# Optimization experiments

Measured on AMD Instinct MI355X. Metric: run time of the kernel, lower is better.

## Reference

```python
import jax, jax.numpy as jnp
import numpy as np


def setup_inputs() -> dict:
    key = jax.random.key(0)
    k1, k2, k3 = jax.random.split(key, 3)
    B, L, D, K = 64, 1024, 768, 1024
    token_embeddings = jax.random.normal(k1, (B, L, D), dtype=jnp.float32)
    gates = jax.random.uniform(k2, (B, L), dtype=jnp.float32)
    attention_mask = jnp.ones((B, L), dtype=jnp.float32)
    centroids = jax.random.normal(k3, (K, D), dtype=jnp.float32)
    return {
        "token_embeddings": token_embeddings,
        "gates": gates,
        "attention_mask": attention_mask,
        "centroids": centroids,
        "entity_cluster": 0,
    }


def reference(token_embeddings, gates, attention_mask, centroids, entity_cluster):
    # ClusterFilter.apply: cdist -> argmin -> entity-cluster gating mask
    B, L, D = token_embeddings.shape
    flat = token_embeddings.reshape(-1, D)                      # [B*L, D]
    # squared Euclidean distances (argmin is invariant to sqrt)
    x2 = jnp.sum(flat * flat, axis=-1, keepdims=True)           # [B*L, 1]
    c2 = jnp.sum(centroids * centroids, axis=-1)                # [K]
    d2 = x2 - 2.0 * (flat @ centroids.T) + c2                   # [B*L, K]
    assignments = jnp.argmin(d2, axis=1).reshape(B, L)          # [B, L]
    entity_mask = (assignments == entity_cluster).astype(gates.dtype)
    entity_mask = entity_mask * attention_mask
    return gates * entity_mask
```

## Files before the change

### kernel.cpp

```cpp
#include <hip/hip_runtime.h>
#include <hip/hip_bf16.h>
#include <stdint.h>

typedef _Float16 half_t;
typedef __attribute__((ext_vector_type(8))) _Float16 half8;
typedef __attribute__((ext_vector_type(4))) _Float16 half4v;
typedef __attribute__((ext_vector_type(4))) float float4v;
typedef unsigned long long u64;

#define D_DIM 768
#define K_CENT 1024
#define M_TOTAL 65536
#define BM 256
#define BN 256
#define BK 32
#define NT 24
#define NTN 4

#define BPLANE 16384u

#define CLO_OFF  (NTN * NT * BPLANE)
#define C2_OFF   (2u * CLO_OFF)
#define PART_OFF (C2_OFF + 8192u)


__device__ __forceinline__ uint32_t swz(uint32_t row, uint32_t kbyte) {
  return (row * 64u + kbyte) ^ (((row >> 1) & 3u) << 4);
}

__device__ __forceinline__ void gll16(const void* g, void* l) {
  __builtin_amdgcn_global_load_lds((const __attribute__((address_space(1))) void*)g,
                                   (__attribute__((address_space(3))) void*)l,
                                   16, 0, 0);
}

__global__ __launch_bounds__(256) void prep_centroids(const float* __restrict__ cent,
                                                      uint8_t* __restrict__ ws) {
  const int n = blockIdx.x;
  const int nt = n >> 8, row = n & 255;
  float ss = 0.f;
  for (int d = threadIdx.x; d < D_DIM; d += 256) {
    float a = cent[n * D_DIM + d];
    ss += a * a;
    half_t hi = (half_t)a;
    half_t lo = (half_t)(a - (float)hi);
    int chunk = d >> 5, k = d & 31;
    uint32_t off = (uint32_t)(nt * NT + chunk) * BPLANE + swz((uint32_t)row, (uint32_t)k * 2u);
    *(half_t*)(ws + off) = hi;
    *(half_t*)(ws + CLO_OFF + off) = lo;
  }
  for (int s = 32; s > 0; s >>= 1) ss += __shfl_down(ss, s, 64);
  __shared__ float red[4];
  if ((threadIdx.x & 63) == 0) red[threadIdx.x >> 6] = ss;
  __syncthreads();
  if (threadIdx.x == 0) {
    float* c2 = (float*)(ws + C2_OFF);
    c2[n] = red[0] + red[1] + red[2] + red[3];
  }
}

__global__ __launch_bounds__(512, 2) void cluster_gemm(const float* __restrict__ X,
                                                       const uint8_t* __restrict__ wsro,
                                                       u64* __restrict__ partial) {
  extern __shared__ uint8_t smem[];

  const int bid = blockIdx.x;
  const int L = (bid & 7) * 128 + (bid >> 3);
  const int m_tile = L >> 2, n_tile = L & 3;
  const int m0 = m_tile * BM;

  const int tid = threadIdx.x;
  const int lane = tid & 63, w = tid >> 6;
  const int wm = w >> 2, wn = w & 3;
  const uint32_t kb = (uint32_t)((lane >> 4) << 4);

  const float* c2p = (const float*)(wsro + C2_OFF);
  const int ncol = n_tile * 256 + wn * 64 + (lane & 15);
  float c2v[4];
#pragma unroll
  for (int n = 0; n < 4; ++n) c2v[n] = c2p[ncol + n * 16];

  float4v acc[8][4];
#pragma unroll
  for (int m = 0; m < 8; ++m)
#pragma unroll
    for (int n = 0; n < 4; ++n) acc[m][n] = (float4v){0.f, 0.f, 0.f, 0.f};

  float4v apf[4];
  half8 ah[4], al[4], bh0[2], bl0[2], bh1[2], bl1[2];

#define A_LOAD(T1) { const int d0 = (T1) * BK;                                        \
  _Pragma("unroll") for (int i = 0; i < 4; ++i) {                                     \
    int f = tid + i * 512; int row = f >> 3, c4 = f & 7;                              \
    apf[i] = *(const float4v*)(X + (size_t)(m0 + row) * D_DIM + d0 + c4 * 4); } }

#define A_WRITE(DB) { _Pragma("unroll") for (int i = 0; i < 4; ++i) {                 \
    int f = tid + i * 512; int row = f >> 3, c4 = f & 7;                              \
    half4v hi, lo;                                                                    \
    _Pragma("unroll") for (int j = 0; j < 4; ++j) {                                   \
      half_t h = (half_t)apf[i][j]; hi[j] = h; lo[j] = (half_t)(apf[i][j] - (float)h);} \
    uint32_t a = (DB) + swz((uint32_t)row, (uint32_t)c4 * 8u);                        \
    *(half4v*)(smem + a) = hi; *(half4v*)(smem + a + 16384u) = lo; } }

#define B_GLL_HI(T1, DB) { const uint8_t* s_ = wsro + (uint32_t)(n_tile * NT + (T1)) * BPLANE; \
    uint32_t o_ = (uint32_t)w * 2048u;                                                \
    gll16(s_ + o_ + (lane << 4), smem + (DB) + o_);                                   \
    gll16(s_ + o_ + 1024u + (lane << 4), smem + (DB) + o_ + 1024u); }

#define B_GLL_LO(T1, DB) { const uint8_t* s_ = wsro + CLO_OFF + (uint32_t)(n_tile * NT + (T1)) * BPLANE; \
    uint32_t o_ = (uint32_t)w * 2048u;                                                \
    gll16(s_ + o_ + (lane << 4), smem + (DB) + 16384u + o_);                          \
    gll16(s_ + o_ + 1024u + (lane << 4), smem + (DB) + 16384u + o_ + 1024u); }

#define READ_A(HALF, AB) { _Pragma("unroll") for (int m = 0; m < 4; ++m) {            \
    uint32_t a = (AB) + swz((uint32_t)(wm * 128 + ((HALF) * 4 + m) * 16 + (lane & 15)), kb); \
    ah[m] = *(const half8*)(smem + a); al[m] = *(const half8*)(smem + a + 16384u); } }

#define READ_B(NH, BB, BH, BL) { _Pragma("unroll") for (int n = 0; n < 2; ++n) {      \
    uint32_t a = (BB) + swz((uint32_t)(wn * 64 + ((NH) * 2 + n) * 16 + (lane & 15)), kb); \
    BH[n] = *(const half8*)(smem + a); BL[n] = *(const half8*)(smem + a + 16384u); } }

#define MFMA_Q(MB, NB, BH, BL) { __builtin_amdgcn_s_setprio(1);                       \
  _Pragma("unroll") for (int m = 0; m < 4; ++m)                                       \
  _Pragma("unroll") for (int n = 0; n < 2; ++n) {                                     \
    float4v* A_ = &acc[(MB) + m][(NB) + n];                                           \
    *A_ = __builtin_amdgcn_mfma_f32_16x16x32_f16(ah[m], BH[n], *A_, 0, 0, 0);         \
    *A_ = __builtin_amdgcn_mfma_f32_16x16x32_f16(ah[m], BL[n], *A_, 0, 0, 0);         \
    *A_ = __builtin_amdgcn_mfma_f32_16x16x32_f16(al[m], BH[n], *A_, 0, 0, 0); }       \
  __builtin_amdgcn_s_setprio(0); }

#define BAR() __builtin_amdgcn_s_barrier()

  uint32_t Ab = 0u, Bb = 65536u;

  A_LOAD(0);
  B_GLL_HI(0, Bb); B_GLL_LO(0, Bb);
  A_WRITE(Ab);
  asm volatile("s_waitcnt vmcnt(0) lgkmcnt(0)" ::: "memory");
  BAR();

  for (int t = 0; t < NT; ++t) {
    const uint32_t AbN = Ab ^ 32768u, BbN = Bb ^ 32768u;
    const bool st = (t + 1 < NT);
    if (st) { A_LOAD(t + 1); B_GLL_HI(t + 1, BbN); }
    READ_A(0, Ab);
    READ_B(0, Bb, bh0, bl0);
    BAR();
    MFMA_Q(0, 0, bh0, bl0);
    BAR();
    if (st) { B_GLL_LO(t + 1, BbN); }
    READ_B(1, Bb, bh1, bl1);
    BAR();
    MFMA_Q(0, 2, bh1, bl1);
    BAR();
    READ_A(1, Ab);
    BAR();
    MFMA_Q(4, 2, bh1, bl1);
    BAR();
    if (st) { A_WRITE(AbN); }
    MFMA_Q(4, 0, bh0, bl0);
    asm volatile("s_waitcnt vmcnt(0) lgkmcnt(0)" ::: "memory");
    BAR();
    Ab = AbN; Bb = BbN;
  }

  u64* scratch = (u64*)smem;
  const int g = lane >> 4;
#pragma unroll
  for (int m = 0; m < 8; ++m) {
#pragma unroll
    for (int r = 0; r < 4; ++r) {
      u64 key = ~0ull;
#pragma unroll
      for (int n = 0; n < 4; ++n) {
        float s = c2v[n] - 2.0f * acc[m][n][r];
        uint32_t ub = __float_as_uint(s);
        ub ^= (uint32_t)((int32_t)ub >> 31) | 0x80000000u;
        u64 cand = ((u64)ub << 32) | (uint32_t)(ncol + n * 16);
        key = cand < key ? cand : key;
      }
#pragma unroll
      for (int d = 1; d < 16; d <<= 1) {
        u64 o = __shfl_xor(key, d, 64);
        key = o < key ? o : key;
      }
      if ((lane & 15) == 0) {
        int row = wm * 128 + m * 16 + g * 4 + r;
        scratch[row * 4 + wn] = key;
      }
    }
  }
  __syncthreads();
  if (tid < 256) {
    u64 k = scratch[tid * 4];
#pragma unroll
    for (int j = 1; j < 4; ++j) { u64 o = scratch[tid * 4 + j]; k = o < k ? o : k; }
    partial[(size_t)(m0 + tid) * NTN + n_tile] = k;
  }
}

__global__ __launch_bounds__(256) void finalize(const u64* __restrict__ partial,
                                                const float* __restrict__ gates,
                                                const float* __restrict__ att,
                                                const int* __restrict__ ecp,
                                                float* __restrict__ out) {
  int r = blockIdx.x * 256 + threadIdx.x;
  const u64* p = partial + (size_t)r * NTN;
  u64 k = p[0];
#pragma unroll
  for (int j = 1; j < NTN; ++j) { u64 o = p[j]; k = o < k ? o : k; }
  int idx = (int)(uint32_t)k;
  out[r] = gates[r] * att[r] * ((idx == *ecp) ? 1.0f : 0.0f);
}

extern "C" void kernel_launch(void* const* d_in, const int* in_sizes, int n_in,
                              void* d_out, int out_size, void* d_ws, size_t ws_size,
                              hipStream_t stream) {
  const float* X     = (const float*)d_in[0];
  const float* gates = (const float*)d_in[1];
  const float* att   = (const float*)d_in[2];
  const float* cent  = (const float*)d_in[3];
  const int*   ec    = (const int*)d_in[4];
  uint8_t* ws = (uint8_t*)d_ws;
  float* out = (float*)d_out;
  u64* partial = (u64*)(ws + PART_OFF);

  hipFuncSetAttribute((const void*)cluster_gemm,
                      hipFuncAttributeMaxDynamicSharedMemorySize, 131072);

  prep_centroids<<<K_CENT, 256, 0, stream>>>(cent, ws);
  cluster_gemm<<<(M_TOTAL / BM) * NTN, 512, 131072, stream>>>(X, ws, partial);
  finalize<<<M_TOTAL / 256, 256, 0, stream>>>(partial, gates, att, ec, out);
}
```

Baseline: 490.5 us.

## Pre-split X into fp16 hi/lo swizzled planes and stream via global_load_lds

```diff
diff --git a/kernel.cpp b/kernel.cpp
--- a/kernel.cpp
+++ b/kernel.cpp
@@ -22,7 +22,10 @@
 #define CLO_OFF  (NTN * NT * BPLANE)
 #define C2_OFF   (2u * CLO_OFF)
 #define PART_OFF (C2_OFF + 8192u)
-
+#define XHI_OFF  8388608u
+#define XPLANE   100663296u
+#define XLO_OFF  (XHI_OFF + XPLANE)
+#define WS_NEED  ((size_t)XLO_OFF + (size_t)XPLANE)
 
 __device__ __forceinline__ uint32_t swz(uint32_t row, uint32_t kbyte) {
   return (row * 64u + kbyte) ^ (((row >> 1) & 3u) << 4);
@@ -33,6 +36,8 @@
                                    (__attribute__((address_space(3))) void*)l,
                                    16, 0, 0);
 }
+
+#define BAR() __builtin_amdgcn_s_barrier()
 
 __global__ __launch_bounds__(256) void prep_centroids(const float* __restrict__ cent,
                                                       uint8_t* __restrict__ ws) {
@@ -59,15 +64,38 @@
   }
 }
 
-__global__ __launch_bounds__(512, 2) void cluster_gemm(const float* __restrict__ X,
-                                                       const uint8_t* __restrict__ wsro,
-                                                       u64* __restrict__ partial) {
+__global__ __launch_bounds__(256) void prep_x(const float* __restrict__ X,
+                                              uint8_t* __restrict__ ws) {
+  const uint32_t bid = blockIdx.x;
+  const uint32_t mt = bid / 24u, ch = bid % 24u;
+  const int tid = threadIdx.x;
+  const int row = tid >> 3, c4 = tid & 7;
+  const uint32_t pbase = (mt * 24u + ch) * BPLANE;
+#pragma unroll
+  for (int i = 0; i < 8; ++i) {
+    int r = row + i * 32;
+    float4v v = *(const float4v*)(X + (size_t)(mt * 256u + r) * D_DIM + ch * 32 + c4 * 4);
+    half4v hi, lo;
+#pragma unroll
+    for (int j = 0; j < 4; ++j) {
+      half_t h = (half_t)v[j];
+      hi[j] = h;
+      lo[j] = (half_t)(v[j] - (float)h);
+    }
+    uint32_t a = pbase + swz((uint32_t)r, (uint32_t)c4 * 8u);
+    *(half4v*)(ws + XHI_OFF + a) = hi;
+    *(half4v*)(ws + XLO_OFF + a) = lo;
+  }
+}
+
+__global__ __launch_bounds__(512, 2) void cluster_gemm_gl(const uint8_t* __restrict__ wsro,
+                                                          u64* __restrict__ partial) {
   extern __shared__ uint8_t smem[];
 
   const int bid = blockIdx.x;
   const int L = (bid & 7) * 128 + (bid >> 3);
-  const int m_tile = L >> 2, n_tile = L & 3;
-  const int m0 = m_tile * BM;
+  const int mt = L >> 2, nt = L & 3;
+  const int m0 = mt * BM;
 
   const int tid = threadIdx.x;
   const int lane = tid & 63, w = tid >> 6;
@@ -75,7 +103,7 @@
   const uint32_t kb = (uint32_t)((lane >> 4) << 4);
 
   const float* c2p = (const float*)(wsro + C2_OFF);
-  const int ncol = n_tile * 256 + wn * 64 + (lane & 15);
+  const int ncol = nt * 256 + wn * 64 + (lane & 15);
   float c2v[4];
 #pragma unroll
   for (int n = 0; n < 4; ++n) c2v[n] = c2p[ncol + n * 16];
@@ -86,38 +114,24 @@
 #pragma unroll
     for (int n = 0; n < 4; ++n) acc[m][n] = (float4v){0.f, 0.f, 0.f, 0.f};
 
-  float4v apf[4];
+  const uint8_t* Ah = wsro + XHI_OFF + (uint32_t)(mt * NT) * BPLANE;
+  const uint8_t* Al = wsro + XLO_OFF + (uint32_t)(mt * NT) * BPLANE;
+  const uint8_t* Bh = wsro + (uint32_t)(nt * NT) * BPLANE;
+  const uint8_t* Bl = wsro + CLO_OFF + (uint32_t)(nt * NT) * BPLANE;
+  const uint32_t wo = (uint32_t)w * 2048u;
+
   half8 ah[4], al[4], bh0[2], bl0[2], bh1[2], bl1[2];
 
-#define A_LOAD(T1) { const int d0 = (T1) * BK;                                        \
-  _Pragma("unroll") for (int i = 0; i < 4; ++i) {                                     \
-    int f = tid + i * 512; int row = f >> 3, c4 = f & 7;                              \
-    apf[i] = *(const float4v*)(X + (size_t)(m0 + row) * D_DIM + d0 + c4 * 4); } }
-
-#define A_WRITE(DB) { _Pragma("unroll") for (int i = 0; i < 4; ++i) {                 \
-    int f = tid + i * 512; int row = f >> 3, c4 = f & 7;                              \
-    half4v hi, lo;                                                                    \
-    _Pragma("unroll") for (int j = 0; j < 4; ++j) {                                   \
-      half_t h = (half_t)apf[i][j]; hi[j] = h; lo[j] = (half_t)(apf[i][j] - (float)h);} \
-    uint32_t a = (DB) + swz((uint32_t)row, (uint32_t)c4 * 8u);                        \
-    *(half4v*)(smem + a) = hi; *(half4v*)(smem + a + 16384u) = lo; } }
-
-#define B_GLL_HI(T1, DB) { const uint8_t* s_ = wsro + (uint32_t)(n_tile * NT + (T1)) * BPLANE; \
-    uint32_t o_ = (uint32_t)w * 2048u;                                                \
-    gll16(s_ + o_ + (lane << 4), smem + (DB) + o_);                                   \
-    gll16(s_ + o_ + 1024u + (lane << 4), smem + (DB) + o_ + 1024u); }
-
-#define B_GLL_LO(T1, DB) { const uint8_t* s_ = wsro + CLO_OFF + (uint32_t)(n_tile * NT + (T1)) * BPLANE; \
-    uint32_t o_ = (uint32_t)w * 2048u;                                                \
-    gll16(s_ + o_ + (lane << 4), smem + (DB) + 16384u + o_);                          \
-    gll16(s_ + o_ + 1024u + (lane << 4), smem + (DB) + 16384u + o_ + 1024u); }
-
-#define READ_A(HALF, AB) { _Pragma("unroll") for (int m = 0; m < 4; ++m) {            \
-    uint32_t a = (AB) + swz((uint32_t)(wm * 128 + ((HALF) * 4 + m) * 16 + (lane & 15)), kb); \
+#define GL_CP(SRC, DOFF) {                                                            \
+    gll16((SRC) + wo + (lane << 4), smem + (DOFF) + wo);                              \
+    gll16((SRC) + wo + 1024u + (lane << 4), smem + (DOFF) + wo + 1024u); }
+
+#define GL_RA(HALF, DB) { _Pragma("unroll") for (int m = 0; m < 4; ++m) {             \
+    uint32_t a = (DB) + swz((uint32_t)(wm * 128 + ((HALF) * 4 + m) * 16 + (lane & 15)), kb); \
     ah[m] = *(const half8*)(smem + a); al[m] = *(const half8*)(smem + a + 16384u); } }
 
-#define READ_B(NH, BB, BH, BL) { _Pragma("unroll") for (int n = 0; n < 2; ++n) {      \
-    uint32_t a = (BB) + swz((uint32_t)(wn * 64 + ((NH) * 2 + n) * 16 + (lane & 15)), kb); \
+#define GL_RB(NH, DB, BH, BL) { _Pragma("unroll") for (int n = 0; n < 2; ++n) {       \
+    uint32_t a = (DB) + 32768u + swz((uint32_t)(wn * 64 + ((NH) * 2 + n) * 16 + (lane & 15)), kb); \
     BH[n] = *(const half8*)(smem + a); BL[n] = *(const half8*)(smem + a + 16384u); } }
 
 #define MFMA_Q(MB, NB, BH, BL) { __builtin_amdgcn_s_setprio(1);                       \
@@ -129,7 +143,131 @@
     *A_ = __builtin_amdgcn_mfma_f32_16x16x32_f16(al[m], BH[n], *A_, 0, 0, 0); }       \
   __builtin_amdgcn_s_setprio(0); }
 
-#define BAR() __builtin_amdgcn_s_barrier()
+  GL_CP(Ah, 0u); GL_CP(Al, 16384u);
+  GL_CP(Bh, 32768u); GL_CP(Bl, 49152u);
+  asm volatile("s_waitcnt vmcnt(0)" ::: "memory");
+  BAR();
+
+  uint32_t cb = 0u;
+  for (int t = 0; t < NT; ++t) {
+    const uint32_t nb = cb ^ 65536u;
+    const bool st = (t + 1 < NT);
+    const uint32_t po = (uint32_t)(t + 1) * BPLANE;
+    if (st) { GL_CP(Ah + po, nb); GL_CP(Al + po, nb + 16384u); }
+    GL_RA(0, cb);
+    GL_RB(0, cb, bh0, bl0);
+    BAR();
+    MFMA_Q(0, 0, bh0, bl0);
+    BAR();
+    if (st) { GL_CP(Bh + po, nb + 32768u); GL_CP(Bl + po, nb + 49152u); }
+    GL_RB(1, cb, bh1, bl1);
+    BAR();
+    MFMA_Q(0, 2, bh1, bl1);
+    BAR();
+    GL_RA(1, cb);
+    BAR();
+    MFMA_Q(4, 2, bh1, bl1);
+    MFMA_Q(4, 0, bh0, bl0);
+    asm volatile("s_waitcnt vmcnt(0)" ::: "memory");
+    BAR();
+    cb = nb;
+  }
+
+  u64* scratch = (u64*)smem;
+  const int g = lane >> 4;
+#pragma unroll
+  for (int m = 0; m < 8; ++m) {
+#pragma unroll
+    for (int r = 0; r < 4; ++r) {
+      u64 key = ~0ull;
+#pragma unroll
+      for (int n = 0; n < 4; ++n) {
+        float s = c2v[n] - 2.0f * acc[m][n][r];
+        uint32_t ub = __float_as_uint(s);
+        ub ^= (uint32_t)((int32_t)ub >> 31) | 0x80000000u;
+        u64 cand = ((u64)ub << 32) | (uint32_t)(ncol + n * 16);
+        key = cand < key ? cand : key;
+      }
+#pragma unroll
+      for (int d = 1; d < 16; d <<= 1) {
+        u64 o = __shfl_xor(key, d, 64);
+        key = o < key ? o : key;
+      }
+      if ((lane & 15) == 0) {
+        int row = wm * 128 + m * 16 + g * 4 + r;
+        scratch[row * 4 + wn] = key;
+      }
+    }
+  }
+  __syncthreads();
+  if (tid < 256) {
+    u64 k = scratch[tid * 4];
+#pragma unroll
+    for (int j = 1; j < 4; ++j) { u64 o = scratch[tid * 4 + j]; k = o < k ? o : k; }
+    partial[(size_t)(m0 + tid) * NTN + nt] = k;
+  }
+}
+
+__global__ __launch_bounds__(512, 2) void cluster_gemm_rs(const float* __restrict__ X,
+                                                          const uint8_t* __restrict__ wsro,
+                                                          u64* __restrict__ partial) {
+  extern __shared__ uint8_t smem[];
+
+  const int bid = blockIdx.x;
+  const int L = (bid & 7) * 128 + (bid >> 3);
+  const int m_tile = L >> 2, n_tile = L & 3;
+  const int m0 = m_tile * BM;
+
+  const int tid = threadIdx.x;
+  const int lane = tid & 63, w = tid >> 6;
+  const int wm = w >> 2, wn = w & 3;
+  const uint32_t kb = (uint32_t)((lane >> 4) << 4);
+
+  const float* c2p = (const float*)(wsro + C2_OFF);
+  const int ncol = n_tile * 256 + wn * 64 + (lane & 15);
+  float c2v[4];
+#pragma unroll
+  for (int n = 0; n < 4; ++n) c2v[n] = c2p[ncol + n * 16];
+
+  float4v acc[8][4];
+#pragma unroll
+  for (int m = 0; m < 8; ++m)
+#pragma unroll
+    for (int n = 0; n < 4; ++n) acc[m][n] = (float4v){0.f, 0.f, 0.f, 0.f};
+
+  float4v apf[4];
+  half8 ah[4], al[4], bh0[2], bl0[2], bh1[2], bl1[2];
+
+#define A_LOAD(T1) { const int d0 = (T1) * BK;                                        \
+  _Pragma("unroll") for (int i = 0; i < 4; ++i) {                                     \
+    int f = tid + i * 512; int row = f >> 3, c4 = f & 7;                              \
+    apf[i] = *(const float4v*)(X + (size_t)(m0 + row) * D_DIM + d0 + c4 * 4); } }
+
+#define A_WRITE(DB) { _Pragma("unroll") for (int i = 0; i < 4; ++i) {                 \
+    int f = tid + i * 512; int row = f >> 3, c4 = f & 7;                              \
+    half4v hi, lo;                                                                    \
+    _Pragma("unroll") for (int j = 0; j < 4; ++j) {                                   \
+      half_t h = (half_t)apf[i][j]; hi[j] = h; lo[j] = (half_t)(apf[i][j] - (float)h);} \
+    uint32_t a = (DB) + swz((uint32_t)row, (uint32_t)c4 * 8u);                        \
+    *(half4v*)(smem + a) = hi; *(half4v*)(smem + a + 16384u) = lo; } }
+
+#define B_GLL_HI(T1, DB) { const uint8_t* s_ = wsro + (uint32_t)(n_tile * NT + (T1)) * BPLANE; \
+    uint32_t o_ = (uint32_t)w * 2048u;                                                \
+    gll16(s_ + o_ + (lane << 4), smem + (DB) + o_);                                   \
+    gll16(s_ + o_ + 1024u + (lane << 4), smem + (DB) + o_ + 1024u); }
+
+#define B_GLL_LO(T1, DB) { const uint8_t* s_ = wsro + CLO_OFF + (uint32_t)(n_tile * NT + (T1)) * BPLANE; \
+    uint32_t o_ = (uint32_t)w * 2048u;                                                \
+    gll16(s_ + o_ + (lane << 4), smem + (DB) + 16384u + o_);                          \
+    gll16(s_ + o_ + 1024u + (lane << 4), smem + (DB) + 16384u + o_ + 1024u); }
+
+#define READ_A(HALF, AB) { _Pragma("unroll") for (int m = 0; m < 4; ++m) {            \
+    uint32_t a = (AB) + swz((uint32_t)(wm * 128 + ((HALF) * 4 + m) * 16 + (lane & 15)), kb); \
+    ah[m] = *(const half8*)(smem + a); al[m] = *(const half8*)(smem + a + 16384u); } }
+
+#define READ_B(NH, BB, BH, BL) { _Pragma("unroll") for (int n = 0; n < 2; ++n) {      \
+    uint32_t a = (BB) + swz((uint32_t)(wn * 64 + ((NH) * 2 + n) * 16 + (lane & 15)), kb); \
+    BH[n] = *(const half8*)(smem + a); BL[n] = *(const half8*)(smem + a + 16384u); } }
 
   uint32_t Ab = 0u, Bb = 65536u;
 
@@ -225,10 +363,17 @@
   float* out = (float*)d_out;
   u64* partial = (u64*)(ws + PART_OFF);
 
-  hipFuncSetAttribute((const void*)cluster_gemm,
+  hipFuncSetAttribute((const void*)cluster_gemm_gl,
                       hipFuncAttributeMaxDynamicSharedMemorySize, 131072);
+  hipFuncSetAttribute((const void*)cluster_gemm_rs,
+                      hipFuncAttributeMaxDynamicSharedMemorySize, 131072);
 
   prep_centroids<<<K_CENT, 256, 0, stream>>>(cent, ws);
-  cluster_gemm<<<(M_TOTAL / BM) * NTN, 512, 131072, stream>>>(X, ws, partial);
+  if (ws_size >= WS_NEED) {
+    prep_x<<<256 * 24, 256, 0, stream>>>(X, ws);
+    cluster_gemm_gl<<<(M_TOTAL / BM) * NTN, 512, 131072, stream>>>(ws, partial);
+  } else {
+    cluster_gemm_rs<<<(M_TOTAL / BM) * NTN, 512, 131072, stream>>>(X, ws, partial);
+  }
   finalize<<<M_TOTAL / 256, 256, 0, stream>>>(partial, gates, att, ec, out);
 }
```

Result: slower. 564.2 us (+15.0%).

## Software-pipeline LDS fragment reads with MFMA and cut barriers per k-step

Applied to the files above, without the earlier changes.

```diff
diff --git a/kernel.cpp b/kernel.cpp
--- a/kernel.cpp
+++ b/kernel.cpp
@@ -33,6 +33,8 @@
                                    (__attribute__((address_space(3))) void*)l,
                                    16, 0, 0);
 }
+
+#define BAR() __builtin_amdgcn_s_barrier()
 
 __global__ __launch_bounds__(256) void prep_centroids(const float* __restrict__ cent,
                                                       uint8_t* __restrict__ ws) {
@@ -87,7 +89,7 @@
     for (int n = 0; n < 4; ++n) acc[m][n] = (float4v){0.f, 0.f, 0.f, 0.f};
 
   float4v apf[4];
-  half8 ah[4], al[4], bh0[2], bl0[2], bh1[2], bl1[2];
+  half8 ah0[4], al0[4], ah1[4], al1[4], bh0[2], bl0[2], bh1[2], bl1[2];
 
 #define A_LOAD(T1) { const int d0 = (T1) * BK;                                        \
   _Pragma("unroll") for (int i = 0; i < 4; ++i) {                                     \
@@ -112,24 +114,22 @@
     gll16(s_ + o_ + (lane << 4), smem + (DB) + 16384u + o_);                          \
     gll16(s_ + o_ + 1024u + (lane << 4), smem + (DB) + 16384u + o_ + 1024u); }
 
-#define READ_A(HALF, AB) { _Pragma("unroll") for (int m = 0; m < 4; ++m) {            \
-    uint32_t a = (AB) + swz((uint32_t)(wm * 128 + ((HALF) * 4 + m) * 16 + (lane & 15)), kb); \
-    ah[m] = *(const half8*)(smem + a); al[m] = *(const half8*)(smem + a + 16384u); } }
+#define READ_A(HALF, AB, AH, AL) { _Pragma("unroll") for (int m = 0; m < 4; ++m) {    \
+    uint32_t a = (AB) + swz((uint32_t)(wm * 128 + (HALF) + m * 16 + (lane & 15)), kb); \
+    AH[m] = *(const half8*)(smem + a); AL[m] = *(const half8*)(smem + a + 16384u); } }
 
 #define READ_B(NH, BB, BH, BL) { _Pragma("unroll") for (int n = 0; n < 2; ++n) {      \
     uint32_t a = (BB) + swz((uint32_t)(wn * 64 + ((NH) * 2 + n) * 16 + (lane & 15)), kb); \
     BH[n] = *(const half8*)(smem + a); BL[n] = *(const half8*)(smem + a + 16384u); } }
 
-#define MFMA_Q(MB, NB, BH, BL) { __builtin_amdgcn_s_setprio(1);                       \
+#define MFMA_Q(MB, NB, AH, AL, BH, BL) { __builtin_amdgcn_s_setprio(1);               \
   _Pragma("unroll") for (int m = 0; m < 4; ++m)                                       \
   _Pragma("unroll") for (int n = 0; n < 2; ++n) {                                     \
     float4v* A_ = &acc[(MB) + m][(NB) + n];                                           \
-    *A_ = __builtin_amdgcn_mfma_f32_16x16x32_f16(ah[m], BH[n], *A_, 0, 0, 0);         \
-    *A_ = __builtin_amdgcn_mfma_f32_16x16x32_f16(ah[m], BL[n], *A_, 0, 0, 0);         \
-    *A_ = __builtin_amdgcn_mfma_f32_16x16x32_f16(al[m], BH[n], *A_, 0, 0, 0); }       \
+    *A_ = __builtin_amdgcn_mfma_f32_16x16x32_f16(AH[m], BH[n], *A_, 0, 0, 0);         \
+    *A_ = __builtin_amdgcn_mfma_f32_16x16x32_f16(AH[m], BL[n], *A_, 0, 0, 0);         \
+    *A_ = __builtin_amdgcn_mfma_f32_16x16x32_f16(AL[m], BH[n], *A_, 0, 0, 0); }       \
   __builtin_amdgcn_s_setprio(0); }
-
-#define BAR() __builtin_amdgcn_s_barrier()
 
   uint32_t Ab = 0u, Bb = 65536u;
 
@@ -138,30 +138,31 @@
   A_WRITE(Ab);
   asm volatile("s_waitcnt vmcnt(0) lgkmcnt(0)" ::: "memory");
   BAR();
+  READ_A(0, Ab, ah0, al0);
+  READ_B(0, Bb, bh0, bl0);
 
   for (int t = 0; t < NT; ++t) {
     const uint32_t AbN = Ab ^ 32768u, BbN = Bb ^ 32768u;
     const bool st = (t + 1 < NT);
-    if (st) { A_LOAD(t + 1); B_GLL_HI(t + 1, BbN); }
-    READ_A(0, Ab);
-    READ_B(0, Bb, bh0, bl0);
-    BAR();
-    MFMA_Q(0, 0, bh0, bl0);
-    BAR();
-    if (st) { B_GLL_LO(t + 1, BbN); }
+    if (st) { A_LOAD(t + 1); }
     READ_B(1, Bb, bh1, bl1);
-    BAR();
-    MFMA_Q(0, 2, bh1, bl1);
-    BAR();
-    READ_A(1, Ab);
-    BAR();
-    MFMA_Q(4, 2, bh1, bl1);
+    MFMA_Q(0, 0, ah0, al0, bh0, bl0);
+    BAR();
+    if (st) { B_GLL_HI(t + 1, BbN); B_GLL_LO(t + 1, BbN); }
+    READ_A(64, Ab, ah1, al1);
+    MFMA_Q(0, 2, ah0, al0, bh1, bl1);
     BAR();
     if (st) { A_WRITE(AbN); }
-    MFMA_Q(4, 0, bh0, bl0);
+    MFMA_Q(4, 2, ah1, al1, bh1, bl1);
+    BAR();
+    MFMA_Q(4, 0, ah1, al1, bh0, bl0);
     asm volatile("s_waitcnt vmcnt(0) lgkmcnt(0)" ::: "memory");
     BAR();
     Ab = AbN; Bb = BbN;
+    if (st) {
+      READ_A(0, Ab, ah0, al0);
+      READ_B(0, Bb, bh0, bl0);
+    }
   }
 
   u64* scratch = (u64*)smem;
```

Measured after the change: 649.4 us. 32.4% more time.
